# Kernel tuning notes

Hardware: AMD Instinct MI355X
Metric: run time of the kernel (lower is better)

## Reference

```python
import jax, jax.numpy as jnp
import numpy as np

B, S, D = 4, 4096, 2048
L = 3  # conv kernel size (L_cache)


def setup_inputs() -> dict:
    key = jax.random.key(0)
    k1, k2, k3, k4 = jax.random.split(key, 4)
    scale_in = 1.0 / np.sqrt(D)
    return {
        "x": jax.random.normal(k1, (B, S, D), dtype=jnp.float32),
        "W_in": jax.random.normal(k2, (D, 3 * D), dtype=jnp.float32) * scale_in,
        "conv_w": jax.random.normal(k3, (D, L), dtype=jnp.float32) * (1.0 / np.sqrt(L)),
        "W_out": jax.random.normal(k4, (D, D), dtype=jnp.float32) * scale_in,
    }


def _causal_depthwise_conv(bx, conv_w):
    # bx: [B, D, S], conv_w: [D, L]; causal cross-correlation per channel
    rhs = conv_w[:, None, :]  # [D, 1, L] = (out_ch, in_ch/groups, width)
    return jax.lax.conv_general_dilated(
        bx, rhs,
        window_strides=(1,),
        padding=[(L - 1, 0)],
        dimension_numbers=("NCH", "OIH", "NCH"),
        feature_group_count=bx.shape[1],
    )


def reference(x, W_in, conv_w, W_out):
    # in_proj: [B,S,D] @ [D,3D] -> [B,S,3D]
    BCx = jnp.einsum("bsd,de->bse", x, W_in)
    B_gate, C_gate, x_proj = jnp.split(BCx, 3, axis=-1)  # each [B,S,D]
    Bx = (B_gate * x_proj).transpose(0, 2, 1)            # [B,D,S]
    conv_out = _causal_depthwise_conv(Bx, conv_w)         # [B,D,S]
    y = C_gate * conv_out.transpose(0, 2, 1)              # [B,S,D]
    return jnp.einsum("bsd,de->bse", y, W_out)            # [B,S,D]
```

## Files before the change

### kernel.cpp

```cpp
#include <hip/hip_runtime.h>
#include <cstddef>
#include <cstdint>

#define D_DIM 2048
#define S_DIM 4096
#define B_DIM 4
#define M_DIM (B_DIM * S_DIM)
#define N1_DIM (3 * D_DIM)

typedef short bf16x8 __attribute__((ext_vector_type(8)));
typedef float f32x4  __attribute__((ext_vector_type(4)));

typedef const unsigned int __attribute__((address_space(1))) gu32_t;
typedef unsigned int       __attribute__((address_space(3))) lu32_t;

__device__ __forceinline__ unsigned short f2bf(float f) {
    unsigned int u = __float_as_uint(f);
    u += 0x7FFFu + ((u >> 16) & 1u);
    return (unsigned short)(u >> 16);
}
__device__ __forceinline__ float bf2f(unsigned short h) {
    return __uint_as_float(((unsigned int)h) << 16);
}

__global__ void k_convert(const float* __restrict__ in, unsigned short* __restrict__ out, int n8) {
    int i = blockIdx.x * blockDim.x + threadIdx.x;
    if (i >= n8) return;
    const float4* p = (const float4*)in + (size_t)i * 2;
    float4 a = p[0];
    float4 b = p[1];
    union { unsigned short s[8]; uint4 v; } r;
    r.s[0] = f2bf(a.x); r.s[1] = f2bf(a.y); r.s[2] = f2bf(a.z); r.s[3] = f2bf(a.w);
    r.s[4] = f2bf(b.x); r.s[5] = f2bf(b.y); r.s[6] = f2bf(b.z); r.s[7] = f2bf(b.w);
    ((uint4*)out)[i] = r.v;
}

__global__ void k_transpose(const float* __restrict__ in, unsigned short* __restrict__ out,
                            int R, int C) {
    __shared__ float t[32][33];
    int c0 = blockIdx.x * 32, r0 = blockIdx.y * 32;
    int x = threadIdx.x;
    for (int yy = threadIdx.y; yy < 32; yy += 8)
        t[yy][x] = in[(size_t)(r0 + yy) * C + c0 + x];
    __syncthreads();
    for (int yy = threadIdx.y; yy < 32; yy += 8)
        out[(size_t)(c0 + yy) * R + r0 + x] = f2bf(t[x][yy]);
}

__device__ __forceinline__ void stage_half(const unsigned short* __restrict__ src,
                                           unsigned short* lds_base,
                                           int rowbase, int half, int k0, int K, int tid) {
    const int wave = tid >> 6;
    #pragma unroll
    for (int l = 0; l < 2; ++l) {
        const int gidx = l * 512 + tid;
        const int row  = gidx >> 3;
        const int gs   = (gidx & 7) ^ (row & 7);
        const unsigned short* g = src + (size_t)(rowbase + half * 128 + row) * K + k0 + gs * 8;
        __builtin_amdgcn_global_load_lds((gu32_t*)g,
            (lu32_t*)(lds_base + half * 8192 + (l * 512 + wave * 64) * 8), 16, 0, 0);
    }
}

template <bool OUT_BF16>
__global__ __launch_bounds__(512, 2)
void k_gemm256(const unsigned short* __restrict__ A, const unsigned short* __restrict__ Bt,
               void* __restrict__ Cp, int N, int K) {
    __shared__ unsigned short As[2][16384];
    __shared__ unsigned short Bs[2][16384];

    const int tid  = threadIdx.x;
    const int wave = tid >> 6;
    const int lane = tid & 63;
    const int wm   = wave >> 2;
    const int wn   = wave & 3;
    const int quad = lane >> 4;
    const int rsel = lane & 15;
    (void)wave;

    const int nbx  = gridDim.x;
    const int nwg  = nbx * gridDim.y;
    const int cpx  = nwg >> 3;
    const int orig = blockIdx.y * nbx + blockIdx.x;
    const int swz  = (orig & 7) * cpx + (orig >> 3);
    const int m0 = (swz / nbx) * 256;
    const int n0 = (swz % nbx) * 256;

    f32x4 acc[8][4] = {};

    const int KT = K >> 6;
    const int NI = KT >> 1;

    stage_half(A,  &As[0][0], m0, 0, 0,  K, tid);
    stage_half(A,  &As[0][0], m0, 1, 0,  K, tid);
    stage_half(Bt, &Bs[0][0], n0, 0, 0,  K, tid);
    stage_half(Bt, &Bs[0][0], n0, 1, 0,  K, tid);
    stage_half(Bt, &Bs[1][0], n0, 0, 64, K, tid);
    stage_half(Bt, &Bs[1][0], n0, 1, 64, K, tid);
    asm volatile("s_waitcnt vmcnt(4)" ::: "memory");
    __builtin_amdgcn_s_barrier();

    for (int i = 0; i < NI; ++i) {
        const int kA  = i << 7;
        const bool nxt = (i + 1 < NI);
        #pragma unroll
        for (int tt = 0; tt < 2; ++tt) {
            const unsigned short* Asl = &As[tt][0];
            const unsigned short* Bsl = &Bs[tt][0];
            bf16x8 bfr[4][2];
            #pragma unroll
            for (int q = 0; q < 4; ++q) {
                bf16x8 af[2][2];
                #pragma unroll
                for (int mi = 0; mi < 2; ++mi) {
                    const int ra = wm * 128 + (q * 2 + mi) * 16 + rsel;
                    #pragma unroll
                    for (int kb = 0; kb < 2; ++kb) {
                        const int g = (kb * 4 + quad) ^ (ra & 7);
                        af[mi][kb] = *(const bf16x8*)&Asl[ra * 64 + g * 8];
                    }
                }
                if (q == 0) {
                    #pragma unroll
                    for (int j = 0; j < 4; ++j) {
                        const int rb = wn * 64 + j * 16 + rsel;
                        #pragma unroll
                        for (int kb = 0; kb < 2; ++kb) {
                            const int g = (kb * 4 + quad) ^ (rb & 7);
                            bfr[j][kb] = *(const bf16x8*)&Bsl[rb * 64 + g * 8];
                        }
                    }
                }
                const int ph = tt * 4 + q;
                switch (ph) {
                    case 0: stage_half(A,  &As[1][0], m0, 0, kA + 64,  K, tid); break;
                    case 1: stage_half(A,  &As[1][0], m0, 1, kA + 64,  K, tid); break;
                    case 2: if (nxt) stage_half(Bt, &Bs[0][0], n0, 0, kA + 128, K, tid); break;
                    case 3: if (nxt) stage_half(Bt, &Bs[0][0], n0, 1, kA + 128, K, tid); break;
                    case 4: if (nxt) stage_half(A,  &As[0][0], m0, 0, kA + 128, K, tid); break;
                    case 5: if (nxt) stage_half(A,  &As[0][0], m0, 1, kA + 128, K, tid); break;
                    case 6: if (nxt) stage_half(Bt, &Bs[1][0], n0, 0, kA + 192, K, tid); break;
                    case 7: if (nxt) stage_half(Bt, &Bs[1][0], n0, 1, kA + 192, K, tid); break;
                }
                __builtin_amdgcn_s_barrier();
                asm volatile("s_waitcnt lgkmcnt(0)" ::: "memory");
                __builtin_amdgcn_s_setprio(1);
                #pragma unroll
                for (int kb = 0; kb < 2; ++kb)
                    #pragma unroll
                    for (int mi = 0; mi < 2; ++mi)
                        #pragma unroll
                        for (int j = 0; j < 4; ++j)
                            acc[q * 2 + mi][j] = __builtin_amdgcn_mfma_f32_16x16x32_bf16(
                                af[mi][kb], bfr[j][kb], acc[q * 2 + mi][j], 0, 0, 0);
                __builtin_amdgcn_s_setprio(0);
                if (ph == 3) {
                    if (nxt) asm volatile("s_waitcnt vmcnt(4)" ::: "memory");
                    else     asm volatile("s_waitcnt vmcnt(0)" ::: "memory");
                } else if (ph == 7) {
                    asm volatile("s_waitcnt vmcnt(4)" ::: "memory");
                }
                __builtin_amdgcn_s_barrier();
            }
        }
    }

    #pragma unroll
    for (int fm = 0; fm < 8; ++fm) {
        #pragma unroll
        for (int j = 0; j < 4; ++j) {
            const int col  = n0 + wn * 64 + j * 16 + rsel;
            const int rowb = m0 + wm * 128 + fm * 16 + quad * 4;
            #pragma unroll
            for (int r = 0; r < 4; ++r) {
                const size_t off = (size_t)(rowb + r) * N + col;
                if (OUT_BF16) ((unsigned short*)Cp)[off] = f2bf(acc[fm][j][r]);
                else          ((float*)Cp)[off] = acc[fm][j][r];
            }
        }
    }
}

__global__ void k_conv_gate(const unsigned short* __restrict__ BCx,
                            const float* __restrict__ conv_w,
                            unsigned short* __restrict__ y) {
    const int bs = blockIdx.x;
    const int s  = bs & (S_DIM - 1);
    const int d0 = threadIdx.x * 8;
    const size_t row = (size_t)bs * N1_DIM;

    union U8 { uint4 v; unsigned short s[8]; };
    float bx_m2[8], bx_m1[8], bx_0[8];
    #pragma unroll
    for (int j = 0; j < 8; ++j) { bx_m2[j] = 0.f; bx_m1[j] = 0.f; }

    U8 g, xp;
    g.v  = *(const uint4*)&BCx[row + d0];
    xp.v = *(const uint4*)&BCx[row + 2 * D_DIM + d0];
    #pragma unroll
    for (int j = 0; j < 8; ++j) bx_0[j] = bf2f(g.s[j]) * bf2f(xp.s[j]);

    if (s >= 1) {
        g.v  = *(const uint4*)&BCx[row - N1_DIM + d0];
        xp.v = *(const uint4*)&BCx[row - N1_DIM + 2 * D_DIM + d0];
        #pragma unroll
        for (int j = 0; j < 8; ++j) bx_m1[j] = bf2f(g.s[j]) * bf2f(xp.s[j]);
    }
    if (s >= 2) {
        g.v  = *(const uint4*)&BCx[row - 2 * N1_DIM + d0];
        xp.v = *(const uint4*)&BCx[row - 2 * N1_DIM + 2 * D_DIM + d0];
        #pragma unroll
        for (int j = 0; j < 8; ++j) bx_m2[j] = bf2f(g.s[j]) * bf2f(xp.s[j]);
    }

    U8 c; c.v = *(const uint4*)&BCx[row + D_DIM + d0];
    U8 r;
    #pragma unroll
    for (int j = 0; j < 8; ++j) {
        const float* w = conv_w + (size_t)(d0 + j) * 3;
        const float conv = w[0] * bx_m2[j] + w[1] * bx_m1[j] + w[2] * bx_0[j];
        r.s[j] = f2bf(bf2f(c.s[j]) * conv);
    }
    *(uint4*)&y[(size_t)bs * D_DIM + d0] = r.v;
}

extern "C" void kernel_launch(void* const* d_in, const int* in_sizes, int n_in,
                              void* d_out, int out_size, void* d_ws, size_t ws_size,
                              hipStream_t stream) {
    const float* x      = (const float*)d_in[0];
    const float* W_in   = (const float*)d_in[1];
    const float* conv_w = (const float*)d_in[2];
    const float* W_out  = (const float*)d_in[3];
    float* out = (float*)d_out;

    char* ws = (char*)d_ws;
    unsigned short* xb     = (unsigned short*)ws;
    unsigned short* Wt_in  = (unsigned short*)(ws + (size_t)67108864);
    unsigned short* Wt_out = (unsigned short*)(ws + (size_t)67108864 + 25165824);
    unsigned short* BCx    = (unsigned short*)(ws + (size_t)67108864 + 25165824 + 8388608);

    const int n8 = M_DIM * D_DIM / 8;
    k_convert<<<dim3((n8 + 255) / 256), 256, 0, stream>>>(x, xb, n8);
    k_transpose<<<dim3(N1_DIM / 32, D_DIM / 32), dim3(32, 8), 0, stream>>>(W_in, Wt_in, D_DIM, N1_DIM);
    k_transpose<<<dim3(D_DIM / 32, D_DIM / 32), dim3(32, 8), 0, stream>>>(W_out, Wt_out, D_DIM, D_DIM);

    k_gemm256<true><<<dim3(N1_DIM / 256, M_DIM / 256), 512, 0, stream>>>(xb, Wt_in, BCx, N1_DIM, D_DIM);
    k_conv_gate<<<dim3(M_DIM), 256, 0, stream>>>(BCx, conv_w, xb );
    k_gemm256<false><<<dim3(D_DIM / 256, M_DIM / 256), 512, 0, stream>>>(xb, Wt_out, out, D_DIM, D_DIM);
}
```

Measured before the change: 873.9 us.

## Reorder GEMM256 half-tile prefetch schedule and use a 128-tile kernel for out-projection

The main 256x256 GEMM now issues eight single-half global-to-LDS loads per iteration, interleaving A and B halves. It waits with a uniform vmcnt(6) every fourth phase and drops the explicit lgkmcnt wait. Warp rows are remapped so each q-phase reads a 64-row slab spanning both wave rows. Instead of skipping the final prefetches, the last iteration reloads the current k-slice. A new simpler single-buffered 128x128 tile GEMM replaces the 256 kernel for the output projection, giving more workgroups but no load/compute overlap.

After: 880.0 us. Within noise of the previous version (+0.7%).

```diff
diff --git a/kernel.cpp b/kernel.cpp
--- a/kernel.cpp
+++ b/kernel.cpp
@@ -47,18 +47,18 @@
         out[(size_t)(c0 + yy) * R + r0 + x] = f2bf(t[x][yy]);
 }
 
-__device__ __forceinline__ void stage_half(const unsigned short* __restrict__ src,
-                                           unsigned short* lds_base,
-                                           int rowbase, int half, int k0, int K, int tid) {
+__device__ __forceinline__ void stage_half2(const unsigned short* __restrict__ src,
+                                            unsigned short* lds_half,
+                                            int growbase, int k0, int K, int tid) {
     const int wave = tid >> 6;
     #pragma unroll
     for (int l = 0; l < 2; ++l) {
         const int gidx = l * 512 + tid;
         const int row  = gidx >> 3;
         const int gs   = (gidx & 7) ^ (row & 7);
-        const unsigned short* g = src + (size_t)(rowbase + half * 128 + row) * K + k0 + gs * 8;
+        const unsigned short* g = src + (size_t)(growbase + row) * K + k0 + gs * 8;
         __builtin_amdgcn_global_load_lds((gu32_t*)g,
-            (lu32_t*)(lds_base + half * 8192 + (l * 512 + wave * 64) * 8), 16, 0, 0);
+            (lu32_t*)(lds_half + (l * 512 + wave * 64) * 8), 16, 0, 0);
     }
 }
 
@@ -70,13 +70,12 @@
     __shared__ unsigned short Bs[2][16384];
 
     const int tid  = threadIdx.x;
+    const int lane = tid & 63;
     const int wave = tid >> 6;
-    const int lane = tid & 63;
     const int wm   = wave >> 2;
     const int wn   = wave & 3;
     const int quad = lane >> 4;
     const int rsel = lane & 15;
-    (void)wave;
 
     const int nbx  = gridDim.x;
     const int nwg  = nbx * gridDim.y;
@@ -91,18 +90,20 @@
     const int KT = K >> 6;
     const int NI = KT >> 1;
 
-    stage_half(A,  &As[0][0], m0, 0, 0,  K, tid);
-    stage_half(A,  &As[0][0], m0, 1, 0,  K, tid);
-    stage_half(Bt, &Bs[0][0], n0, 0, 0,  K, tid);
-    stage_half(Bt, &Bs[0][0], n0, 1, 0,  K, tid);
-    stage_half(Bt, &Bs[1][0], n0, 0, 64, K, tid);
-    stage_half(Bt, &Bs[1][0], n0, 1, 64, K, tid);
-    asm volatile("s_waitcnt vmcnt(4)" ::: "memory");
+    stage_half2(A,  &As[0][0],        m0,       0,  K, tid);
+    stage_half2(Bt, &Bs[0][0],        n0,       0,  K, tid);
+    stage_half2(Bt, &Bs[0][0] + 8192, n0 + 128, 0,  K, tid);
+    stage_half2(A,  &As[0][0] + 8192, m0 + 128, 0,  K, tid);
+    stage_half2(Bt, &Bs[1][0],        n0,       64, K, tid);
+    stage_half2(A,  &As[1][0],        m0,       64, K, tid);
+    stage_half2(Bt, &Bs[1][0] + 8192, n0 + 128, 64, K, tid);
+    asm volatile("s_waitcnt vmcnt(6)" ::: "memory");
     __builtin_amdgcn_s_barrier();
 
     for (int i = 0; i < NI; ++i) {
         const int kA  = i << 7;
-        const bool nxt = (i + 1 < NI);
+        const int kS0 = (i + 1 < NI) ? kA + 128 : kA;
+        const int kS1 = (i + 1 < NI) ? kA + 192 : kA;
         #pragma unroll
         for (int tt = 0; tt < 2; ++tt) {
             const unsigned short* Asl = &As[tt][0];
@@ -113,7 +114,7 @@
                 bf16x8 af[2][2];
                 #pragma unroll
                 for (int mi = 0; mi < 2; ++mi) {
-                    const int ra = wm * 128 + (q * 2 + mi) * 16 + rsel;
+                    const int ra = q * 64 + wm * 32 + mi * 16 + rsel;
                     #pragma unroll
                     for (int kb = 0; kb < 2; ++kb) {
                         const int g = (kb * 4 + quad) ^ (ra & 7);
@@ -133,17 +134,16 @@
                 }
                 const int ph = tt * 4 + q;
                 switch (ph) {
-                    case 0: stage_half(A,  &As[1][0], m0, 0, kA + 64,  K, tid); break;
-                    case 1: stage_half(A,  &As[1][0], m0, 1, kA + 64,  K, tid); break;
-                    case 2: if (nxt) stage_half(Bt, &Bs[0][0], n0, 0, kA + 128, K, tid); break;
-                    case 3: if (nxt) stage_half(Bt, &Bs[0][0], n0, 1, kA + 128, K, tid); break;
-                    case 4: if (nxt) stage_half(A,  &As[0][0], m0, 0, kA + 128, K, tid); break;
-                    case 5: if (nxt) stage_half(A,  &As[0][0], m0, 1, kA + 128, K, tid); break;
-                    case 6: if (nxt) stage_half(Bt, &Bs[1][0], n0, 0, kA + 192, K, tid); break;
-                    case 7: if (nxt) stage_half(Bt, &Bs[1][0], n0, 1, kA + 192, K, tid); break;
+                    case 0: stage_half2(A,  &As[1][0] + 8192, m0 + 128, kA + 64, K, tid); break;
+                    case 1: stage_half2(Bt, &Bs[0][0],        n0,       kS0,     K, tid); break;
+                    case 2: stage_half2(A,  &As[0][0],        m0,       kS0,     K, tid); break;
+                    case 3: stage_half2(Bt, &Bs[0][0] + 8192, n0 + 128, kS0,     K, tid); break;
+                    case 4: stage_half2(A,  &As[0][0] + 8192, m0 + 128, kS0,     K, tid); break;
+                    case 5: stage_half2(Bt, &Bs[1][0],        n0,       kS1,     K, tid); break;
+                    case 6: stage_half2(A,  &As[1][0],        m0,       kS1,     K, tid); break;
+                    case 7: stage_half2(Bt, &Bs[1][0] + 8192, n0 + 128, kS1,     K, tid); break;
                 }
                 __builtin_amdgcn_s_barrier();
-                asm volatile("s_waitcnt lgkmcnt(0)" ::: "memory");
                 __builtin_amdgcn_s_setprio(1);
                 #pragma unroll
                 for (int kb = 0; kb < 2; ++kb)
@@ -154,12 +154,7 @@
                             acc[q * 2 + mi][j] = __builtin_amdgcn_mfma_f32_16x16x32_bf16(
                                 af[mi][kb], bfr[j][kb], acc[q * 2 + mi][j], 0, 0, 0);
                 __builtin_amdgcn_s_setprio(0);
-                if (ph == 3) {
-                    if (nxt) asm volatile("s_waitcnt vmcnt(4)" ::: "memory");
-                    else     asm volatile("s_waitcnt vmcnt(0)" ::: "memory");
-                } else if (ph == 7) {
-                    asm volatile("s_waitcnt vmcnt(4)" ::: "memory");
-                }
+                if (q == 3) asm volatile("s_waitcnt vmcnt(6)" ::: "memory");
                 __builtin_amdgcn_s_barrier();
             }
         }
@@ -170,12 +165,86 @@
         #pragma unroll
         for (int j = 0; j < 4; ++j) {
             const int col  = n0 + wn * 64 + j * 16 + rsel;
-            const int rowb = m0 + wm * 128 + fm * 16 + quad * 4;
+            const int rowb = m0 + (fm >> 1) * 64 + wm * 32 + (fm & 1) * 16 + quad * 4;
             #pragma unroll
             for (int r = 0; r < 4; ++r) {
                 const size_t off = (size_t)(rowb + r) * N + col;
                 if (OUT_BF16) ((unsigned short*)Cp)[off] = f2bf(acc[fm][j][r]);
                 else          ((float*)Cp)[off] = acc[fm][j][r];
+            }
+        }
+    }
+}
+
+template <bool OUT_BF16>
+__global__ __launch_bounds__(256, 2)
+void k_gemm128(const unsigned short* __restrict__ A, const unsigned short* __restrict__ Bt,
+               void* __restrict__ Cp, int N, int K) {
+    __shared__ unsigned short As[128 * 64];
+    __shared__ unsigned short Bs[128 * 64];
+
+    const int tid  = threadIdx.x;
+    const int wave = tid >> 6;
+    const int lane = tid & 63;
+    const int m0 = blockIdx.y * 128;
+    const int n0 = blockIdx.x * 128;
+    const int wm = (wave & 1) * 64;
+    const int wn = (wave >> 1) * 64;
+
+    f32x4 acc[4][4] = {};
+
+    const int srow = lane >> 3;
+    const int gd   = lane & 7;
+    const int quad = lane >> 4;
+    const int rsel = lane & 15;
+
+    const int KT = K >> 6;
+    for (int kt = 0; kt < KT; ++kt) {
+        const int k0 = kt << 6;
+        __syncthreads();
+        #pragma unroll
+        for (int i = 0; i < 4; ++i) {
+            const int seg = i * 4 + wave;
+            const int row = seg * 8 + srow;
+            const int gs  = gd ^ (row & 7);
+            const unsigned short* ga = A  + (size_t)(m0 + row) * K + k0 + gs * 8;
+            const unsigned short* gb = Bt + (size_t)(n0 + row) * K + k0 + gs * 8;
+            __builtin_amdgcn_global_load_lds((gu32_t*)ga, (lu32_t*)(As + seg * 512), 16, 0, 0);
+            __builtin_amdgcn_global_load_lds((gu32_t*)gb, (lu32_t*)(Bs + seg * 512), 16, 0, 0);
+        }
+        __syncthreads();
+
+        #pragma unroll
+        for (int kb = 0; kb < 2; ++kb) {
+            bf16x8 af[4], bfr[4];
+            #pragma unroll
+            for (int i = 0; i < 4; ++i) {
+                const int ra = wm + i * 16 + rsel;
+                const int ga = (kb * 4 + quad) ^ (ra & 7);
+                af[i] = *(const bf16x8*)&As[ra * 64 + ga * 8];
+                const int rb = wn + i * 16 + rsel;
+                const int gb = (kb * 4 + quad) ^ (rb & 7);
+                bfr[i] = *(const bf16x8*)&Bs[rb * 64 + gb * 8];
+            }
+            #pragma unroll
+            for (int i = 0; i < 4; ++i)
+                #pragma unroll
+                for (int j = 0; j < 4; ++j)
+                    acc[i][j] = __builtin_amdgcn_mfma_f32_16x16x32_bf16(af[i], bfr[j], acc[i][j], 0, 0, 0);
+        }
+    }
+
+    #pragma unroll
+    for (int i = 0; i < 4; ++i) {
+        #pragma unroll
+        for (int j = 0; j < 4; ++j) {
+            const int col  = n0 + wn + j * 16 + rsel;
+            const int rowb = m0 + wm + i * 16 + quad * 4;
+            #pragma unroll
+            for (int r = 0; r < 4; ++r) {
+                const size_t off = (size_t)(rowb + r) * N + col;
+                if (OUT_BF16) ((unsigned short*)Cp)[off] = f2bf(acc[i][j][r]);
+                else          ((float*)Cp)[off] = acc[i][j][r];
             }
         }
     }
@@ -246,5 +315,5 @@
 
     k_gemm256<true><<<dim3(N1_DIM / 256, M_DIM / 256), 512, 0, stream>>>(xb, Wt_in, BCx, N1_DIM, D_DIM);
     k_conv_gate<<<dim3(M_DIM), 256, 0, stream>>>(BCx, conv_w, xb );
-    k_gemm256<false><<<dim3(D_DIM / 256, M_DIM / 256), 512, 0, stream>>>(xb, Wt_out, out, D_DIM, D_DIM);
-}
+    k_gemm128<false><<<dim3(D_DIM / 128, M_DIM / 128), 256, 0, stream>>>(xb, Wt_out, out, D_DIM, D_DIM);
+}
```
